# Kernel tuning notes

Measured on AMD Instinct MI355X. Metric: run time of the kernel, lower is better.

The kernel has to match this reference:

```python
import jax, jax.numpy as jnp
import numpy as np

WINDOW_SIZE = 512
NUM_HEADS = 16
HIDDEN = 1024
HEAD_DIM = HIDDEN // NUM_HEADS
SCALING = HEAD_DIM ** (-0.5)


def sliding_window_mask(seq_len, window_size):
    # row i attends to cols j with i - w//2 <= j <= i + w//2 (clipped to bounds)
    i = jnp.arange(seq_len)[:, None]
    j = jnp.arange(seq_len)[None, :]
    half = window_size // 2
    return jnp.abs(i - j) <= half  # [S, S] bool


def setup_inputs() -> dict:
    key = jax.random.key(0)
    k0, k1, k2, k3, k4 = jax.random.split(key, 5)
    B, S = 2, 2048
    hidden_states = jax.random.normal(k0, (B, S, HIDDEN), dtype=jnp.float32)
    scale = 0.02
    Wq = jax.random.normal(k1, (HIDDEN, HIDDEN), dtype=jnp.float32) * scale
    Wk = jax.random.normal(k2, (HIDDEN, HIDDEN), dtype=jnp.float32) * scale
    Wv = jax.random.normal(k3, (HIDDEN, HIDDEN), dtype=jnp.float32) * scale
    Wo = jax.random.normal(k4, (HIDDEN, HIDDEN), dtype=jnp.float32) * scale
    return {"hidden_states": hidden_states, "Wq": Wq, "Wk": Wk, "Wv": Wv, "Wo": Wo}


def reference(hidden_states, Wq, Wk, Wv, Wo):
    B, S, _ = hidden_states.shape
    # nn.Linear(bias=False): y = x @ W.T
    def proj(x, W):
        y = jnp.einsum('bsh,oh->bso', x, W)
        return y.reshape(B, S, NUM_HEADS, HEAD_DIM).transpose(0, 2, 1, 3)  # [B,H,S,D]

    q = proj(hidden_states, Wq)
    k = proj(hidden_states, Wk)
    v = proj(hidden_states, Wv)

    mask = sliding_window_mask(S, WINDOW_SIZE)  # [S,S]
    scores = jnp.einsum('bhsd,bhtd->bhst', q, k) * SCALING  # [B,H,S,S]
    scores = jnp.where(mask[None, None], scores, -jnp.inf)
    attn = jax.nn.softmax(scores, axis=-1)
    out = jnp.einsum('bhst,bhtd->bhsd', attn, v)
    out = out.transpose(0, 2, 1, 3).reshape(B, S, HIDDEN)
    out = jnp.einsum('bsh,oh->bso', out, Wo)
    return out, attn
```

## Files before the change

### kernel.cpp

```cpp
#include <hip/hip_runtime.h>

typedef unsigned short u16;
typedef __attribute__((ext_vector_type(8))) __bf16 bf16x8;
typedef __attribute__((ext_vector_type(4))) float f32x4;

#define DEV __device__ __forceinline__
#define SEQ 2048
#define SWZ(r) ((((r) & 7)) ^ (((r) >> 3) & 7))

DEV void async16(void* lds, const void* gptr) {
  __builtin_amdgcn_global_load_lds(
      (const __attribute__((address_space(1))) unsigned int*)gptr,
      (__attribute__((address_space(3))) unsigned int*)lds, 16, 0, 0);
}

DEV u16 f2bf(float x) {
  unsigned u = __float_as_uint(x);
  return (u16)((u + 0x7fffu + ((u >> 16) & 1u)) >> 16);
}

DEV f32x4 mfma(bf16x8 a, bf16x8 b, f32x4 c) {
  return __builtin_amdgcn_mfma_f32_16x16x32_bf16(a, b, c, 0, 0, 0);
}

__global__ __launch_bounds__(256) void k_cvt_all(
    const float* __restrict__ hs, const float* __restrict__ wq,
    const float* __restrict__ wk, const float* __restrict__ wv,
    const float* __restrict__ wo, u16* __restrict__ X16,
    u16* __restrict__ W16) {
  int b = blockIdx.x;
  const float* src;
  u16* dst;
  int off;
  if (b < 4096) {
    src = hs;
    dst = X16;
    off = b * 1024;
  } else {
    int b2 = b - 4096;
    int w = b2 >> 10;
    src = (w == 0) ? wq : (w == 1) ? wk : (w == 2) ? wv : wo;
    dst = W16 + (size_t)w * 1048576;
    off = (b2 & 1023) * 1024;
  }
  int i = off + threadIdx.x * 4;
  float4 v = *(const float4*)(src + i);
  *(ushort4*)(dst + i) = make_ushort4(f2bf(v.x), f2bf(v.y), f2bf(v.z), f2bf(v.w));
}

DEV void gemm_mainloop(const u16* __restrict__ A, const u16* __restrict__ B,
                       int K, u16* As, u16* Bs, f32x4 (&acc)[4][4], int tid) {
  const int wid = tid >> 6, lane = tid & 63;
  const int wm = wid >> 1, wn = wid & 1;
  const int quad = lane >> 4, l15 = lane & 15;
  const int ci0 = tid, ci1 = tid + 256;
  const int r0 = ci0 >> 2, g0 = (ci0 & 3) ^ (r0 & 3);
  const int r1 = ci1 >> 2, g1 = (ci1 & 3) ^ (r1 & 3);
  u16* ldsA0 = As + wid * 512;
  u16* ldsA1 = As + wid * 512 + 2048;
  u16* ldsB0 = Bs + wid * 512;
  u16* ldsB1 = Bs + wid * 512 + 2048;

  for (int k0 = 0; k0 < K; k0 += 32) {
    __syncthreads();
    async16(ldsA0, A + (size_t)r0 * K + k0 + g0 * 8);
    async16(ldsA1, A + (size_t)r1 * K + k0 + g1 * 8);
    async16(ldsB0, B + (size_t)r0 * K + k0 + g0 * 8);
    async16(ldsB1, B + (size_t)r1 * K + k0 + g1 * 8);
    __syncthreads();
    bf16x8 af[4], bf[4];
#pragma unroll
    for (int mt = 0; mt < 4; ++mt) {
      int row = wm * 64 + mt * 16 + l15;
      af[mt] = *(const bf16x8*)(As + row * 32 + (quad ^ (row & 3)) * 8);
    }
#pragma unroll
    for (int nt = 0; nt < 4; ++nt) {
      int row = wn * 64 + nt * 16 + l15;
      bf[nt] = *(const bf16x8*)(Bs + row * 32 + (quad ^ (row & 3)) * 8);
    }
#pragma unroll
    for (int mt = 0; mt < 4; ++mt)
#pragma unroll
      for (int nt = 0; nt < 4; ++nt)
        acc[mt][nt] = mfma(af[mt], bf[nt], acc[mt][nt]);
  }
}

__global__ __launch_bounds__(256) void k_gemm_qkv(
    const u16* __restrict__ X, const u16* __restrict__ Wq,
    const u16* __restrict__ Wk, const u16* __restrict__ Wv,
    u16* __restrict__ Q16, u16* __restrict__ K16, u16* __restrict__ V16) {
  __shared__ u16 As[128 * 32], Bs[128 * 32];
  const int tid = threadIdx.x;
  const int bm = blockIdx.x, bn = blockIdx.y, z = blockIdx.z;
  const u16* B = (z == 0) ? Wq : (z == 1) ? Wk : Wv;
  u16* dst = (z == 0) ? Q16 : (z == 1) ? K16 : V16;
  const float sc = (z == 0) ? 0.125f : 1.0f;
  f32x4 acc[4][4];
#pragma unroll
  for (int i = 0; i < 4; ++i)
#pragma unroll
    for (int j = 0; j < 4; ++j) acc[i][j] = (f32x4){0.f, 0.f, 0.f, 0.f};
  gemm_mainloop(X + (size_t)bm * 128 * 1024, B + (size_t)bn * 128 * 1024, 1024,
                As, Bs, acc, tid);
  const int wid = tid >> 6, lane = tid & 63;
  const int wm = wid >> 1, wn = wid & 1, quad = lane >> 4, l15 = lane & 15;
#pragma unroll
  for (int mt = 0; mt < 4; ++mt)
#pragma unroll
    for (int nt = 0; nt < 4; ++nt)
#pragma unroll
      for (int r = 0; r < 4; ++r) {
        int row = bm * 128 + wm * 64 + mt * 16 + quad * 4 + r;
        int col = bn * 128 + wn * 64 + nt * 16 + l15;
        int b = row >> 11, s = row & 2047, h = col >> 6, d = col & 63;
        int bh = b * 16 + h;
        dst[((size_t)bh * SEQ + s) * 64 + d] = f2bf(acc[mt][nt][r] * sc);
      }
}

__global__ __launch_bounds__(256) void k_gemm_out(const u16* __restrict__ A,
                                                  const u16* __restrict__ Bw,
                                                  float* __restrict__ out) {
  __shared__ u16 As[64 * 32], Bs[128 * 32];
  const int tid = threadIdx.x;
  const int wid = tid >> 6, lane = tid & 63;
  const int wm = wid >> 1, wn = wid & 1;
  const int quad = lane >> 4, l15 = lane & 15;
  const int rA = tid >> 2, gA = (tid & 3) ^ (rA & 3);
  const int r1 = (tid + 256) >> 2, g1 = ((tid + 256) & 3) ^ (r1 & 3);
  const u16* Ab = A + (size_t)blockIdx.x * 64 * 1024;
  const u16* Bb = Bw + (size_t)blockIdx.y * 128 * 1024;
  f32x4 acc[2][4];
#pragma unroll
  for (int i = 0; i < 2; ++i)
#pragma unroll
    for (int j = 0; j < 4; ++j) acc[i][j] = (f32x4){0.f, 0.f, 0.f, 0.f};

  for (int k0 = 0; k0 < 1024; k0 += 32) {
    __syncthreads();
    async16(As + wid * 512, Ab + (size_t)rA * 1024 + k0 + gA * 8);
    async16(Bs + wid * 512, Bb + (size_t)rA * 1024 + k0 + gA * 8);
    async16(Bs + wid * 512 + 2048, Bb + (size_t)r1 * 1024 + k0 + g1 * 8);
    __syncthreads();
    bf16x8 af[2], bf[4];
#pragma unroll
    for (int mt = 0; mt < 2; ++mt) {
      int row = wm * 32 + mt * 16 + l15;
      af[mt] = *(const bf16x8*)(As + row * 32 + (quad ^ (row & 3)) * 8);
    }
#pragma unroll
    for (int nt = 0; nt < 4; ++nt) {
      int row = wn * 64 + nt * 16 + l15;
      bf[nt] = *(const bf16x8*)(Bs + row * 32 + (quad ^ (row & 3)) * 8);
    }
#pragma unroll
    for (int mt = 0; mt < 2; ++mt)
#pragma unroll
      for (int nt = 0; nt < 4; ++nt)
        acc[mt][nt] = mfma(af[mt], bf[nt], acc[mt][nt]);
  }
#pragma unroll
  for (int mt = 0; mt < 2; ++mt)
#pragma unroll
    for (int nt = 0; nt < 4; ++nt)
#pragma unroll
      for (int r = 0; r < 4; ++r) {
        int row = blockIdx.x * 64 + wm * 32 + mt * 16 + quad * 4 + r;
        int col = blockIdx.y * 128 + wn * 64 + nt * 16 + l15;
        out[(size_t)row * 1024 + col] = acc[mt][nt][r];
      }
}

__global__ __launch_bounds__(256, 2) void k_attn(
    const u16* __restrict__ Q16, const u16* __restrict__ K16,
    const u16* __restrict__ V16, float* __restrict__ attn_out,
    u16* __restrict__ O16) {
  __shared__ union alignas(16) U {
    struct {
      u16 Qt[4096];
      u16 Kt[2][4096];
      u16 Vt[2][4096];
      u16 P[2][64 * 72];
    } s;
    float Pf[64 * 68];
  } sm;
  __shared__ float rowsum[64];

  const int tid = threadIdx.x, wid = tid >> 6, lane = tid & 63;
  const int quad = lane >> 4, l15 = lane & 15;
  const int qbase = blockIdx.x * 64;
  const int bh = blockIdx.y;
  const int b = bh >> 4, h = bh & 15;
  const u16* Qb = Q16 + ((size_t)bh * SEQ + qbase) * 64;
  const u16* Kb = K16 + (size_t)bh * SEQ * 64;
  const u16* Vb = V16 + (size_t)bh * SEQ * 64;
  float* attn_b = attn_out + (size_t)bh * SEQ * SEQ;

  const int r0 = tid >> 3, g0 = (tid & 7) ^ SWZ(r0);
  const int r1 = r0 + 32, g1 = (tid & 7) ^ SWZ(r1);

  const int tlo = qbase >= 256 ? 0 : (256 - qbase) >> 6;
  const int thi_raw = (SEQ - 64 - qbase + 256) >> 6;
  const int thi = thi_raw > 8 ? 8 : thi_raw;

  async16(sm.s.Qt + wid * 512, Qb + r0 * 64 + g0 * 8);
  async16(sm.s.Qt + wid * 512 + 2048, Qb + (size_t)r1 * 64 + g1 * 8);
  {
    int jb = qbase - 256 + tlo * 64;
    u16* Kd = sm.s.Kt[tlo & 1];
    u16* Vd = sm.s.Vt[tlo & 1];
    async16(Kd + wid * 512, Kb + (size_t)(jb + r0) * 64 + g0 * 8);
    async16(Kd + wid * 512 + 2048, Kb + (size_t)(jb + r1) * 64 + g1 * 8);
    async16(Vd + wid * 512, Vb + (size_t)(jb + r0) * 64 + g0 * 8);
    async16(Vd + wid * 512 + 2048, Vb + (size_t)(jb + r1) * 64 + g1 * 8);
  }
  if (tid < 64) rowsum[tid] = 0.f;

  float racc[4][4];
  f32x4 oacc[4];
#pragma unroll
  for (int mt = 0; mt < 4; ++mt) {
    oacc[mt] = (f32x4){0.f, 0.f, 0.f, 0.f};
#pragma unroll
    for (int r = 0; r < 4; ++r) racc[mt][r] = 0.f;
  }
  unsigned stash[9][8];
  bf16x8 bv_prev[2];
  bf16x8 aq[4][2];
  bool aq_loaded = false;
  const int d = wid * 16 + l15;

#pragma unroll
  for (int t = 0; t < 9; ++t) {
    if (t < tlo || t > thi) continue;
    const int jbase = qbase - 256 + t * 64;
    __syncthreads();
    if (t < thi) {
      int jb = jbase + 64;
      u16* Kd = sm.s.Kt[(t + 1) & 1];
      u16* Vd = sm.s.Vt[(t + 1) & 1];
      async16(Kd + wid * 512, Kb + (size_t)(jb + r0) * 64 + g0 * 8);
      async16(Kd + wid * 512 + 2048, Kb + (size_t)(jb + r1) * 64 + g1 * 8);
      async16(Vd + wid * 512, Vb + (size_t)(jb + r0) * 64 + g0 * 8);
      async16(Vd + wid * 512 + 2048, Vb + (size_t)(jb + r1) * 64 + g1 * 8);
    }
    if (!aq_loaded) {
      aq_loaded = true;
#pragma unroll
      for (int mt = 0; mt < 4; ++mt)
#pragma unroll
        for (int ks = 0; ks < 2; ++ks) {
          int row = mt * 16 + l15;
          aq[mt][ks] = *(const bf16x8*)(sm.s.Qt + row * 64 +
                                        (((ks * 4 + quad) ^ SWZ(row)) * 8));
        }
    }
    if (t > tlo) {
      const u16* Pp = sm.s.P[(t + 1) & 1];
#pragma unroll
      for (int mt = 0; mt < 4; ++mt) {
        int row = mt * 16 + l15;
        bf16x8 ap0 = *(const bf16x8*)(Pp + row * 72 + quad * 8);
        bf16x8 ap1 = *(const bf16x8*)(Pp + row * 72 + 32 + quad * 8);
        oacc[mt] = mfma(ap0, bv_prev[0], oacc[mt]);
        oacc[mt] = mfma(ap1, bv_prev[1], oacc[mt]);
      }
    }
    const u16* Kt = sm.s.Kt[t & 1];
    const u16* Vtp = sm.s.Vt[t & 1];
    bf16x8 bq[2];
#pragma unroll
    for (int ks = 0; ks < 2; ++ks) {
      int row = wid * 16 + l15;
      bq[ks] = *(const bf16x8*)(Kt + row * 64 + (((ks * 4 + quad) ^ SWZ(row)) * 8));
    }
#pragma unroll
    for (int ks = 0; ks < 2; ++ks)
#pragma unroll
      for (int jj = 0; jj < 8; ++jj) {
        int j = ks * 32 + quad * 8 + jj;
        int slot = (d >> 3) ^ SWZ(j);
        bv_prev[ks][jj] = *(const __bf16*)(Vtp + j * 64 + slot * 8 + (d & 7));
      }
    u16* Pc = sm.s.P[t & 1];
    const int jcol = jbase + wid * 16 + l15;
#pragma unroll
    for (int mt = 0; mt < 4; ++mt) {
      f32x4 c = (f32x4){0.f, 0.f, 0.f, 0.f};
      c = mfma(aq[mt][0], bq[0], c);
      c = mfma(aq[mt][1], bq[1], c);
      unsigned p0 = 0, p1 = 0;
#pragma unroll
      for (int r = 0; r < 4; ++r) {
        int i_ = qbase + mt * 16 + quad * 4 + r;
        int dlt = i_ - jcol;
        dlt = dlt < 0 ? -dlt : dlt;
        float e = 0.f;
        if (dlt <= 256) e = __expf(c[r]);
        racc[mt][r] += e;
        unsigned eb = f2bf(e);
        Pc[(mt * 16 + quad * 4 + r) * 72 + wid * 16 + l15] = (u16)eb;
        if (r == 0) p0 = eb;
        if (r == 1) p0 |= eb << 16;
        if (r == 2) p1 = eb;
        if (r == 3) p1 |= eb << 16;
      }
      stash[t][mt * 2] = p0;
      stash[t][mt * 2 + 1] = p1;
    }
  }
  __syncthreads();
  {
    const u16* Pp = sm.s.P[thi & 1];
#pragma unroll
    for (int mt = 0; mt < 4; ++mt) {
      int row = mt * 16 + l15;
      bf16x8 ap0 = *(const bf16x8*)(Pp + row * 72 + quad * 8);
      bf16x8 ap1 = *(const bf16x8*)(Pp + row * 72 + 32 + quad * 8);
      oacc[mt] = mfma(ap0, bv_prev[0], oacc[mt]);
      oacc[mt] = mfma(ap1, bv_prev[1], oacc[mt]);
    }
  }

#pragma unroll
  for (int mt = 0; mt < 4; ++mt)
#pragma unroll
    for (int r = 0; r < 4; ++r) {
      float v = racc[mt][r];
      v += __shfl_xor(v, 1, 16);
      v += __shfl_xor(v, 2, 16);
      v += __shfl_xor(v, 4, 16);
      v += __shfl_xor(v, 8, 16);
      racc[mt][r] = v;
    }
  if (l15 == 0) {
#pragma unroll
    for (int mt = 0; mt < 4; ++mt)
#pragma unroll
      for (int r = 0; r < 4; ++r)
        atomicAdd(&rowsum[mt * 16 + quad * 4 + r], racc[mt][r]);
  }
  __syncthreads();
  float linv[4][4];
#pragma unroll
  for (int mt = 0; mt < 4; ++mt)
#pragma unroll
    for (int r = 0; r < 4; ++r)
      linv[mt][r] = 1.0f / rowsum[mt * 16 + quad * 4 + r];

#pragma unroll
  for (int mt = 0; mt < 4; ++mt)
#pragma unroll
    for (int r = 0; r < 4; ++r) {
      int i_ = qbase + mt * 16 + quad * 4 + r;
      O16[((size_t)b * SEQ + i_) * 1024 + h * 64 + d] =
          f2bf(oacc[mt][r] * linv[mt][r]);
    }

  const int wcol = (tid & 15) * 4, wrow = tid >> 4;
#pragma unroll
  for (int t = 0; t < 9; ++t) {
    if (t < tlo || t > thi) continue;
    const int jbase = qbase - 256 + t * 64;
    __syncthreads();
#pragma unroll
    for (int mt = 0; mt < 4; ++mt) {
      unsigned p0 = stash[t][mt * 2], p1 = stash[t][mt * 2 + 1];
      int rb = mt * 16 + quad * 4;
      int cc = wid * 16 + l15;
      sm.Pf[(rb + 0) * 68 + cc] = __uint_as_float(p0 << 16) * linv[mt][0];
      sm.Pf[(rb + 1) * 68 + cc] = __uint_as_float(p0 & 0xffff0000u) * linv[mt][1];
      sm.Pf[(rb + 2) * 68 + cc] = __uint_as_float(p1 << 16) * linv[mt][2];
      sm.Pf[(rb + 3) * 68 + cc] = __uint_as_float(p1 & 0xffff0000u) * linv[mt][3];
    }
    __syncthreads();
#pragma unroll
    for (int k = 0; k < 4; ++k) {
      int row = wrow + k * 16;
      f32x4 v = *(const f32x4*)(sm.Pf + row * 68 + wcol);
      __builtin_nontemporal_store(
          v, (f32x4*)(attn_b + (size_t)(qbase + row) * SEQ + jbase + wcol));
    }
  }
}

extern "C" void kernel_launch(void* const* d_in, const int* in_sizes, int n_in,
                              void* d_out, int out_size, void* d_ws,
                              size_t ws_size, hipStream_t stream) {
  const float* hs = (const float*)d_in[0];
  const float* Wq = (const float*)d_in[1];
  const float* Wk = (const float*)d_in[2];
  const float* Wv = (const float*)d_in[3];
  const float* Wo = (const float*)d_in[4];
  float* out = (float*)d_out;
  float* attn = out + (size_t)4194304;

  u16* X16 = (u16*)d_ws;
  u16* Wq16 = X16 + 4194304;
  u16* Wk16 = Wq16 + 1048576;
  u16* Wv16 = Wk16 + 1048576;
  u16* Wo16 = Wv16 + 1048576;
  u16* Q16 = Wo16 + 1048576;
  u16* K16 = Q16 + 4194304;
  u16* V16 = K16 + 4194304;
  u16* O16 = V16 + 4194304;

  k_cvt_all<<<8192, 256, 0, stream>>>(hs, Wq, Wk, Wv, Wo, X16, Wq16);
  k_gemm_qkv<<<dim3(32, 8, 3), 256, 0, stream>>>(X16, Wq16, Wk16, Wv16, Q16,
                                                 K16, V16);
  k_attn<<<dim3(32, 32), 256, 0, stream>>>(Q16, K16, V16, attn, O16);
  k_gemm_out<<<dim3(64, 8), 256, 0, stream>>>(O16, Wo16, out);
}
```

Before: 578.8 us.

## Double-buffer GEMM LDS tiles and store attention probabilities directly from registers

Both projection GEMMs now use two LDS buffers, so the async global-to-LDS load of the next K-slice is issued before computing on the current one, dropping one barrier per iteration. The attention kernel no longer stages normalized probabilities through a float LDS tile (the union is removed). Instead each lane writes its own scalar probability values to global memory with nontemporal stores. This removes two barriers per key tile in the epilogue, at the cost of narrower 4-byte writes that coalesce less well than the previous float4 row stores, plus higher LDS use in the GEMMs.

```diff
diff --git a/kernel.cpp b/kernel.cpp
--- a/kernel.cpp
+++ b/kernel.cpp
@@ -48,36 +48,40 @@
   *(ushort4*)(dst + i) = make_ushort4(f2bf(v.x), f2bf(v.y), f2bf(v.z), f2bf(v.w));
 }
 
-DEV void gemm_mainloop(const u16* __restrict__ A, const u16* __restrict__ B,
-                       int K, u16* As, u16* Bs, f32x4 (&acc)[4][4], int tid) {
+DEV void gemm_mainloop_db(const u16* __restrict__ A, const u16* __restrict__ B,
+                          int K, u16* As, u16* Bs, f32x4 (&acc)[4][4],
+                          int tid) {
   const int wid = tid >> 6, lane = tid & 63;
   const int wm = wid >> 1, wn = wid & 1;
   const int quad = lane >> 4, l15 = lane & 15;
-  const int ci0 = tid, ci1 = tid + 256;
-  const int r0 = ci0 >> 2, g0 = (ci0 & 3) ^ (r0 & 3);
-  const int r1 = ci1 >> 2, g1 = (ci1 & 3) ^ (r1 & 3);
-  u16* ldsA0 = As + wid * 512;
-  u16* ldsA1 = As + wid * 512 + 2048;
-  u16* ldsB0 = Bs + wid * 512;
-  u16* ldsB1 = Bs + wid * 512 + 2048;
-
-  for (int k0 = 0; k0 < K; k0 += 32) {
+  const int r0 = tid >> 2, g0 = (tid & 3) ^ (r0 & 3);
+  const int r1 = (tid + 256) >> 2, g1 = ((tid + 256) & 3) ^ (r1 & 3);
+
+  auto stage = [&](int buf, int k0) {
+    u16* a = As + buf * 4096;
+    u16* b = Bs + buf * 4096;
+    async16(a + wid * 512, A + (size_t)r0 * K + k0 + g0 * 8);
+    async16(a + wid * 512 + 2048, A + (size_t)r1 * K + k0 + g1 * 8);
+    async16(b + wid * 512, B + (size_t)r0 * K + k0 + g0 * 8);
+    async16(b + wid * 512 + 2048, B + (size_t)r1 * K + k0 + g1 * 8);
+  };
+  stage(0, 0);
+  const int nk = K >> 5;
+  for (int t = 0; t < nk; ++t) {
     __syncthreads();
-    async16(ldsA0, A + (size_t)r0 * K + k0 + g0 * 8);
-    async16(ldsA1, A + (size_t)r1 * K + k0 + g1 * 8);
-    async16(ldsB0, B + (size_t)r0 * K + k0 + g0 * 8);
-    async16(ldsB1, B + (size_t)r1 * K + k0 + g1 * 8);
-    __syncthreads();
+    if (t + 1 < nk) stage((t + 1) & 1, (t + 1) * 32);
+    const u16* a = As + (t & 1) * 4096;
+    const u16* b = Bs + (t & 1) * 4096;
     bf16x8 af[4], bf[4];
 #pragma unroll
     for (int mt = 0; mt < 4; ++mt) {
       int row = wm * 64 + mt * 16 + l15;
-      af[mt] = *(const bf16x8*)(As + row * 32 + (quad ^ (row & 3)) * 8);
+      af[mt] = *(const bf16x8*)(a + row * 32 + (quad ^ (row & 3)) * 8);
     }
 #pragma unroll
     for (int nt = 0; nt < 4; ++nt) {
       int row = wn * 64 + nt * 16 + l15;
-      bf[nt] = *(const bf16x8*)(Bs + row * 32 + (quad ^ (row & 3)) * 8);
+      bf[nt] = *(const bf16x8*)(b + row * 32 + (quad ^ (row & 3)) * 8);
     }
 #pragma unroll
     for (int mt = 0; mt < 4; ++mt)
@@ -91,7 +95,7 @@
     const u16* __restrict__ X, const u16* __restrict__ Wq,
     const u16* __restrict__ Wk, const u16* __restrict__ Wv,
     u16* __restrict__ Q16, u16* __restrict__ K16, u16* __restrict__ V16) {
-  __shared__ u16 As[128 * 32], Bs[128 * 32];
+  __shared__ u16 As[2 * 4096], Bs[2 * 4096];
   const int tid = threadIdx.x;
   const int bm = blockIdx.x, bn = blockIdx.y, z = blockIdx.z;
   const u16* B = (z == 0) ? Wq : (z == 1) ? Wk : Wv;
@@ -102,8 +106,8 @@
   for (int i = 0; i < 4; ++i)
 #pragma unroll
     for (int j = 0; j < 4; ++j) acc[i][j] = (f32x4){0.f, 0.f, 0.f, 0.f};
-  gemm_mainloop(X + (size_t)bm * 128 * 1024, B + (size_t)bn * 128 * 1024, 1024,
-                As, Bs, acc, tid);
+  gemm_mainloop_db(X + (size_t)bm * 128 * 1024, B + (size_t)bn * 128 * 1024,
+                   1024, As, Bs, acc, tid);
   const int wid = tid >> 6, lane = tid & 63;
   const int wm = wid >> 1, wn = wid & 1, quad = lane >> 4, l15 = lane & 15;
 #pragma unroll
@@ -123,7 +127,7 @@
 __global__ __launch_bounds__(256) void k_gemm_out(const u16* __restrict__ A,
                                                   const u16* __restrict__ Bw,
                                                   float* __restrict__ out) {
-  __shared__ u16 As[64 * 32], Bs[128 * 32];
+  __shared__ u16 As[2 * 2048], Bs[2 * 4096];
   const int tid = threadIdx.x;
   const int wid = tid >> 6, lane = tid & 63;
   const int wm = wid >> 1, wn = wid & 1;
@@ -138,22 +142,28 @@
 #pragma unroll
     for (int j = 0; j < 4; ++j) acc[i][j] = (f32x4){0.f, 0.f, 0.f, 0.f};
 
-  for (int k0 = 0; k0 < 1024; k0 += 32) {
+  auto stage = [&](int buf, int k0) {
+    async16(As + buf * 2048 + wid * 512, Ab + (size_t)rA * 1024 + k0 + gA * 8);
+    async16(Bs + buf * 4096 + wid * 512, Bb + (size_t)rA * 1024 + k0 + gA * 8);
+    async16(Bs + buf * 4096 + wid * 512 + 2048,
+            Bb + (size_t)r1 * 1024 + k0 + g1 * 8);
+  };
+  stage(0, 0);
+  for (int t = 0; t < 32; ++t) {
     __syncthreads();
-    async16(As + wid * 512, Ab + (size_t)rA * 1024 + k0 + gA * 8);
-    async16(Bs + wid * 512, Bb + (size_t)rA * 1024 + k0 + gA * 8);
-    async16(Bs + wid * 512 + 2048, Bb + (size_t)r1 * 1024 + k0 + g1 * 8);
-    __syncthreads();
+    if (t + 1 < 32) stage((t + 1) & 1, (t + 1) * 32);
+    const u16* a = As + (t & 1) * 2048;
+    const u16* b = Bs + (t & 1) * 4096;
     bf16x8 af[2], bf[4];
 #pragma unroll
     for (int mt = 0; mt < 2; ++mt) {
       int row = wm * 32 + mt * 16 + l15;
-      af[mt] = *(const bf16x8*)(As + row * 32 + (quad ^ (row & 3)) * 8);
+      af[mt] = *(const bf16x8*)(a + row * 32 + (quad ^ (row & 3)) * 8);
     }
 #pragma unroll
     for (int nt = 0; nt < 4; ++nt) {
       int row = wn * 64 + nt * 16 + l15;
-      bf[nt] = *(const bf16x8*)(Bs + row * 32 + (quad ^ (row & 3)) * 8);
+      bf[nt] = *(const bf16x8*)(b + row * 32 + (quad ^ (row & 3)) * 8);
     }
 #pragma unroll
     for (int mt = 0; mt < 2; ++mt)
@@ -177,15 +187,10 @@
     const u16* __restrict__ Q16, const u16* __restrict__ K16,
     const u16* __restrict__ V16, float* __restrict__ attn_out,
     u16* __restrict__ O16) {
-  __shared__ union alignas(16) U {
-    struct {
-      u16 Qt[4096];
-      u16 Kt[2][4096];
-      u16 Vt[2][4096];
-      u16 P[2][64 * 72];
-    } s;
-    float Pf[64 * 68];
-  } sm;
+  __shared__ u16 Qt[4096];
+  __shared__ u16 Kt[2][4096];
+  __shared__ u16 Vt[2][4096];
+  __shared__ u16 P[2][64 * 72];
   __shared__ float rowsum[64];
 
   const int tid = threadIdx.x, wid = tid >> 6, lane = tid & 63;
@@ -205,12 +210,12 @@
   const int thi_raw = (SEQ - 64 - qbase + 256) >> 6;
   const int thi = thi_raw > 8 ? 8 : thi_raw;
 
-  async16(sm.s.Qt + wid * 512, Qb + r0 * 64 + g0 * 8);
-  async16(sm.s.Qt + wid * 512 + 2048, Qb + (size_t)r1 * 64 + g1 * 8);
+  async16(Qt + wid * 512, Qb + r0 * 64 + g0 * 8);
+  async16(Qt + wid * 512 + 2048, Qb + (size_t)r1 * 64 + g1 * 8);
   {
     int jb = qbase - 256 + tlo * 64;
-    u16* Kd = sm.s.Kt[tlo & 1];
-    u16* Vd = sm.s.Vt[tlo & 1];
+    u16* Kd = Kt[tlo & 1];
+    u16* Vd = Vt[tlo & 1];
     async16(Kd + wid * 512, Kb + (size_t)(jb + r0) * 64 + g0 * 8);
     async16(Kd + wid * 512 + 2048, Kb + (size_t)(jb + r1) * 64 + g1 * 8);
     async16(Vd + wid * 512, Vb + (size_t)(jb + r0) * 64 + g0 * 8);
@@ -239,8 +244,8 @@
     __syncthreads();
     if (t < thi) {
       int jb = jbase + 64;
-      u16* Kd = sm.s.Kt[(t + 1) & 1];
-      u16* Vd = sm.s.Vt[(t + 1) & 1];
+      u16* Kd = Kt[(t + 1) & 1];
+      u16* Vd = Vt[(t + 1) & 1];
       async16(Kd + wid * 512, Kb + (size_t)(jb + r0) * 64 + g0 * 8);
       async16(Kd + wid * 512 + 2048, Kb + (size_t)(jb + r1) * 64 + g1 * 8);
       async16(Vd + wid * 512, Vb + (size_t)(jb + r0) * 64 + g0 * 8);
@@ -253,12 +258,12 @@
 #pragma unroll
         for (int ks = 0; ks < 2; ++ks) {
           int row = mt * 16 + l15;
-          aq[mt][ks] = *(const bf16x8*)(sm.s.Qt + row * 64 +
+          aq[mt][ks] = *(const bf16x8*)(Qt + row * 64 +
                                         (((ks * 4 + quad) ^ SWZ(row)) * 8));
         }
     }
     if (t > tlo) {
-      const u16* Pp = sm.s.P[(t + 1) & 1];
+      const u16* Pp = P[(t + 1) & 1];
 #pragma unroll
       for (int mt = 0; mt < 4; ++mt) {
         int row = mt * 16 + l15;
@@ -268,13 +273,14 @@
         oacc[mt] = mfma(ap1, bv_prev[1], oacc[mt]);
       }
     }
-    const u16* Kt = sm.s.Kt[t & 1];
-    const u16* Vtp = sm.s.Vt[t & 1];
+    const u16* Ktc = Kt[t & 1];
+    const u16* Vtc = Vt[t & 1];
     bf16x8 bq[2];
 #pragma unroll
     for (int ks = 0; ks < 2; ++ks) {
       int row = wid * 16 + l15;
-      bq[ks] = *(const bf16x8*)(Kt + row * 64 + (((ks * 4 + quad) ^ SWZ(row)) * 8));
+      bq[ks] =
+          *(const bf16x8*)(Ktc + row * 64 + (((ks * 4 + quad) ^ SWZ(row)) * 8));
     }
 #pragma unroll
     for (int ks = 0; ks < 2; ++ks)
@@ -282,9 +288,9 @@
       for (int jj = 0; jj < 8; ++jj) {
         int j = ks * 32 + quad * 8 + jj;
         int slot = (d >> 3) ^ SWZ(j);
-        bv_prev[ks][jj] = *(const __bf16*)(Vtp + j * 64 + slot * 8 + (d & 7));
-      }
-    u16* Pc = sm.s.P[t & 1];
+        bv_prev[ks][jj] = *(const __bf16*)(Vtc + j * 64 + slot * 8 + (d & 7));
+      }
+    u16* Pc = P[t & 1];
     const int jcol = jbase + wid * 16 + l15;
 #pragma unroll
     for (int mt = 0; mt < 4; ++mt) {
@@ -313,7 +319,7 @@
   }
   __syncthreads();
   {
-    const u16* Pp = sm.s.P[thi & 1];
+    const u16* Pp = P[thi & 1];
 #pragma unroll
     for (int mt = 0; mt < 4; ++mt) {
       int row = mt * 16 + l15;
@@ -359,31 +365,21 @@
           f2bf(oacc[mt][r] * linv[mt][r]);
     }
 
-  const int wcol = (tid & 15) * 4, wrow = tid >> 4;
-#pragma unroll
-  for (int t = 0; t < 9; ++t) {
-    if (t < tlo || t > thi) continue;
-    const int jbase = qbase - 256 + t * 64;
-    __syncthreads();
-#pragma unroll
-    for (int mt = 0; mt < 4; ++mt) {
-      unsigned p0 = stash[t][mt * 2], p1 = stash[t][mt * 2 + 1];
-      int rb = mt * 16 + quad * 4;
-      int cc = wid * 16 + l15;
-      sm.Pf[(rb + 0) * 68 + cc] = __uint_as_float(p0 << 16) * linv[mt][0];
-      sm.Pf[(rb + 1) * 68 + cc] = __uint_as_float(p0 & 0xffff0000u) * linv[mt][1];
-      sm.Pf[(rb + 2) * 68 + cc] = __uint_as_float(p1 << 16) * linv[mt][2];
-      sm.Pf[(rb + 3) * 68 + cc] = __uint_as_float(p1 & 0xffff0000u) * linv[mt][3];
-    }
-    __syncthreads();
-#pragma unroll
-    for (int k = 0; k < 4; ++k) {
-      int row = wrow + k * 16;
-      f32x4 v = *(const f32x4*)(sm.Pf + row * 68 + wcol);
-      __builtin_nontemporal_store(
-          v, (f32x4*)(attn_b + (size_t)(qbase + row) * SEQ + jbase + wcol));
-    }
-  }
+#pragma unroll
+  for (int mt = 0; mt < 4; ++mt)
+#pragma unroll
+    for (int r = 0; r < 4; ++r) {
+      int i_ = qbase + mt * 16 + quad * 4 + r;
+      float* p = attn_b + (size_t)i_ * SEQ + (qbase - 256) + d;
+#pragma unroll
+      for (int t = 0; t < 9; ++t) {
+        if (t < tlo || t > thi) continue;
+        unsigned pk = stash[t][mt * 2 + (r >> 1)];
+        unsigned bits = (r & 1) ? (pk & 0xffff0000u) : (pk << 16);
+        __builtin_nontemporal_store(__uint_as_float(bits) * linv[mt][r],
+                                    p + t * 64);
+      }
+    }
 }
 
 extern "C" void kernel_launch(void* const* d_in, const int* in_sizes, int n_in,
```

New measurement: 586.2 us. About the same (+1.3%).
